# Kernel tuning notes

Hardware: AMD Instinct MI355X
Metric: run time of the kernel (lower is better)

Reference implementation:

```python
import jax, jax.numpy as jnp
import numpy as np
from jax import lax

# constants mirroring init_kwargs
WORD_MIN_SCORE = 0.5
CHAR_MIN_SCORE = 0.25
WORD_STRIDE = 4
CHAR_STRIDE = 4
WORD_NMS_IOU = 0.3
CHAR_NMS_IOU = 0.3
K_WORD = 512   # fixed candidate budget for word NMS (jit-friendly stand-in for dynamic np.where)
K_CHAR = 2048  # fixed candidate budget for char NMS
H_MAP = 512
W_MAP = 512
NUM_CHAR_CLASS = 68


def _oriented_boxes(tblr, orient, scale_w, scale_h, stride):
    # vectorized rotate_rect over every pixel: rect corners (x-l, y-t, x+r, y+b)
    # rotated by angle `orient` around anchor (x, y), all in image coords.
    _, H, W = tblr.shape
    ys, xs = jnp.meshgrid(jnp.arange(H, dtype=tblr.dtype), jnp.arange(W, dtype=tblr.dtype), indexing='ij')
    t, b, l, r = tblr[0], tblr[1], tblr[2], tblr[3]
    sw = scale_w * stride
    sh = scale_h * stride
    x1 = sw * (xs - l); x2 = sw * (xs + r)
    y1 = sh * (ys - t); y2 = sh * (ys + b)
    ax = sw * xs; ay = sh * ys
    cx = jnp.stack([x1, x2, x2, x1], axis=-1)  # [H,W,4]
    cy = jnp.stack([y1, y1, y2, y2], axis=-1)
    c = jnp.cos(orient)[..., None]
    s = jnp.sin(orient)[..., None]
    dx = cx - ax[..., None]
    dy = cy - ay[..., None]
    rx = ax[..., None] + dx * c - dy * s
    ry = ay[..., None] + dx * s + dy * c
    pts = jnp.stack([rx, ry], axis=-1).reshape(H, W, 8)  # x0,y0,...,x3,y3
    return pts.reshape(-1, 8)


def _nms_keep(pts, scores, iou_thresh):
    # pts [K,8] already sorted by descending score; greedy NMS on axis-aligned
    # envelopes of the oriented boxes (fixed-shape stand-in for polygon IoU).
    xs = pts[:, 0::2]; ys = pts[:, 1::2]
    x1 = xs.min(1); x2 = xs.max(1)
    y1 = ys.min(1); y2 = ys.max(1)
    area = jnp.maximum(x2 - x1, 0.0) * jnp.maximum(y2 - y1, 0.0)
    ix1 = jnp.maximum(x1[:, None], x1[None, :])
    iy1 = jnp.maximum(y1[:, None], y1[None, :])
    ix2 = jnp.minimum(x2[:, None], x2[None, :])
    iy2 = jnp.minimum(y2[:, None], y2[None, :])
    inter = jnp.maximum(ix2 - ix1, 0.0) * jnp.maximum(iy2 - iy1, 0.0)
    iou = inter / (area[:, None] + area[None, :] - inter + 1e-6)
    K = pts.shape[0]
    ar = jnp.arange(K)

    def body(i, keep):
        sup = keep[i] & (iou[i] > iou_thresh) & (ar > i)
        return keep & ~sup

    keep = lax.fori_loop(0, K, body, jnp.ones((K,), dtype=bool))
    return keep & (scores > 0.0)


def _clip_round(pts, W, H):
    out = jnp.round(pts)
    x = jnp.clip(out[:, 0::2], 0.0, W - 1.0)
    y = jnp.clip(out[:, 1::2], 0.0, H - 1.0)
    return jnp.stack([x, y], axis=-1).reshape(pts.shape)


def setup_inputs() -> dict:
    key = jax.random.key(0)
    k = jax.random.split(key, 6)
    return {
        'pred_word_fg': jax.random.uniform(k[0], (H_MAP, W_MAP), dtype=jnp.float32),
        'pred_word_tblr': jax.random.uniform(k[1], (4, H_MAP, W_MAP), dtype=jnp.float32) * 4.0,
        'pred_word_orient': jax.random.normal(k[2], (H_MAP, W_MAP), dtype=jnp.float32) * 0.3,
        'pred_char_fg': jax.random.uniform(k[3], (H_MAP, W_MAP), dtype=jnp.float32),
        'pred_char_tblr': jax.random.uniform(k[4], (4, H_MAP, W_MAP), dtype=jnp.float32) * 2.0,
        'pred_char_cls': jax.random.uniform(k[5], (NUM_CHAR_CLASS, H_MAP, W_MAP), dtype=jnp.float32),
        'im_scale_w': 1,
        'im_scale_h': 1,
        'original_im_w': 2048,
        'original_im_h': 2048,
    }


def reference(pred_word_fg, pred_word_tblr, pred_word_orient, pred_char_fg,
              pred_char_tblr, pred_char_cls, im_scale_w, im_scale_h,
              original_im_w, original_im_h):
    sw = float(im_scale_w); sh = float(im_scale_h)
    # ---- parse_word_bboxes ----
    word_pts = _oriented_boxes(pred_word_tblr, pred_word_orient, sw, sh, WORD_STRIDE)
    word_mask = (pred_word_fg > WORD_MIN_SCORE).reshape(-1)
    word_scores = jnp.where(word_mask, pred_word_fg.reshape(-1), 0.0)
    ws, widx = lax.top_k(word_scores, K_WORD)
    wpts = word_pts[widx]
    wkeep = _nms_keep(wpts, ws, WORD_NMS_IOU)
    wpts = _clip_round(wpts, original_im_w, original_im_h)
    word_bboxes = jnp.concatenate([wpts, ws[:, None]], axis=1)  # [K_WORD, 9]
    # ---- parse_char_torch (orientation fixed at 0) ----
    char_pts = _oriented_boxes(pred_char_tblr, jnp.zeros_like(pred_char_fg), sw, sh, CHAR_STRIDE)
    char_mask = word_mask & (pred_char_fg > CHAR_MIN_SCORE).reshape(-1)
    char_fg_scores = jnp.where(char_mask, pred_char_fg.reshape(-1), 0.0)
    cs, cidx = lax.top_k(char_fg_scores, K_CHAR)
    cpts = char_pts[cidx]
    ckeep = _nms_keep(cpts, cs, CHAR_NMS_IOU)
    cpts = _clip_round(cpts, original_im_w, original_im_h)
    char_bboxes = jnp.concatenate([cpts, cs[:, None]], axis=1)  # [K_CHAR, 9]
    C = pred_char_cls.shape[0]
    cls_flat = pred_char_cls.reshape(C, -1).T  # [H*W, C]
    char_scores = cls_flat[cidx]               # [K_CHAR, C]
    return (char_bboxes, char_scores, word_bboxes, wkeep, ckeep)
```

## Files before the change

### kernel.cpp

```cpp
#include <hip/hip_runtime.h>
#include <stdint.h>

typedef unsigned long long u64;
typedef unsigned int u32;

#define N_PIX (512*512)
#define KW 512
#define KC 2048
#define CAPW 4096
#define CAPC 4096
#define NUM_CLS 68
#define WORD_THR 0.5f
#define CHAR_THR 0.25f
#define IOU_THR 0.3f
#define NBLK 128
#define BS 512
#define GSZ (NBLK*BS)
#define LKW 256
#define LKC 256
#define BASE16W 0x3F00u
#define BASE16C 0x3E80u

struct SelState { u64 prefix; u32 kRem; u32 counter; u32 hist[256]; };

__device__ __forceinline__ u64 mk_key(u32 fb, u32 i){
  return (((u64)fb) << 32) | (u64)(0xFFFFFFFFu - i);
}

__global__ void k0_init(SelState* stW, SelState* stC, u32* bars){
  int t = threadIdx.x;
  if (t==0){ stW->prefix=0ull; stW->kRem=KW; stW->counter=0u; }
  if (t==1){ stC->prefix=0ull; stC->kRem=KC; stC->counter=0u; }
  if (t < 8) bars[t] = 0u;
  stW->hist[t]=0u; stC->hist[t]=0u;
}

__device__ __forceinline__ void scan_wave(SelState* st, u32 base16, int lane){
  u32 h[4];
  #pragma unroll
  for (int q=0;q<4;q++)
    h[q] = __hip_atomic_load(&st->hist[lane*4+q], __ATOMIC_RELAXED, __HIP_MEMORY_SCOPE_AGENT);
  u32 lsum = h[0]+h[1]+h[2]+h[3];
  u32 v = lsum;
  #pragma unroll
  for (int off=1; off<64; off<<=1){
    u32 t2 = __shfl_down(v, off, 64);
    if (lane + off < 64) v += t2;
  }
  u32 above = v - lsum;
  u32 k = st->kRem;
  u32 sfx1 = h[3]+h[2]+h[1], sfx2 = h[3]+h[2], sfx3 = h[3];
  int best = -1;
  if      (above + sfx3 >= k) best = lane*4+3;
  else if (above + sfx2 >= k) best = lane*4+2;
  else if (above + sfx1 >= k) best = lane*4+1;
  else if (above + lsum >= k) best = lane*4+0;
  u64 m = __ballot(best >= 0);
  int d = 0;
  if (m != 0ull){
    int hi_lane = 63 - __clzll(m);
    d = __shfl(best, hi_lane, 64);
  }
  if (lane==0)
    __hip_atomic_store(&st->prefix, ((u64)(base16 + (u32)d)) << 48,
                       __ATOMIC_RELAXED, __HIP_MEMORY_SCOPE_AGENT);
}

__global__ __launch_bounds__(BS)
void k1_hist(const float* __restrict__ wfg, const float* __restrict__ cfg,
             SelState* stW, SelState* stC, u32* bars, u32* ranks){
  __shared__ u32 hW[256], hC[256];
  __shared__ int isLast;
  const int tid = threadIdx.x;
  const int gtid = blockIdx.x*BS + tid;
  const int lane = tid & 63;
  if (gtid < CAPW+CAPC) ranks[gtid] = 0u;
  if (tid < 256){ hW[tid]=0u; hC[tid]=0u; }
  __syncthreads();
  float4 wv4 = ((const float4*)wfg)[gtid];
  float4 cv4 = ((const float4*)cfg)[gtid];
  #pragma unroll
  for (int q=0;q<4;q++){
    float wf = q==0?wv4.x:(q==1?wv4.y:(q==2?wv4.z:wv4.w));
    float cf = q==0?cv4.x:(q==1?cv4.y:(q==2?cv4.z:cv4.w));
    bool wp = wf > WORD_THR;
    if (wp) atomicAdd(&hW[(__float_as_uint(wf)>>16) - BASE16W], 1u);
    if (wp && cf > CHAR_THR) atomicAdd(&hC[(__float_as_uint(cf)>>16) - BASE16C], 1u);
  }
  __syncthreads();
  if (tid < 256){
    if (hW[tid]) atomicAdd(&stW->hist[tid], hW[tid]);
    if (hC[tid]) atomicAdd(&stC->hist[tid], hC[tid]);
  }
  __syncthreads();
  if (tid==0){
    u32 p = __hip_atomic_fetch_add(&bars[0],1u,__ATOMIC_ACQ_REL,__HIP_MEMORY_SCOPE_AGENT);
    isLast = (p == NBLK-1);
  }
  __syncthreads();
  if (isLast && tid < 128){
    if (tid < 64) scan_wave(stW, BASE16W, lane);
    else          scan_wave(stC, BASE16C, lane);
  }
}

__global__ __launch_bounds__(BS)
void k2_compact(const float* __restrict__ wfg, const float* __restrict__ cfg,
                SelState* stW, SelState* stC, u64* candW, u64* candC){
  __shared__ u64 lkW[LKW], lkC[LKC];
  __shared__ u32 lcW, lcC, baseW, baseC;
  const int tid = threadIdx.x;
  const int gtid = blockIdx.x*BS + tid;
  const int lane = tid & 63;
  const u64 lmlt = (1ull << lane) - 1ull;
  if (tid==0){ lcW = 0u; lcC = 0u; }
  __syncthreads();
  u64 tW = stW->prefix, tC = stC->prefix;
  float4 wv4 = ((const float4*)wfg)[gtid];
  float4 cv4 = ((const float4*)cfg)[gtid];
  #pragma unroll
  for (int q=0;q<4;q++){
    float wf = q==0?wv4.x:(q==1?wv4.y:(q==2?wv4.z:wv4.w));
    float cf = q==0?cv4.x:(q==1?cv4.y:(q==2?cv4.z:cv4.w));
    u32 i = 4u*(u32)gtid + (u32)q;
    bool wp = wf > WORD_THR;
    u64 kWd = mk_key(__float_as_uint(wf), i);
    bool pw = wp && (kWd >= tW);
    u64 mW = __ballot(pw);
    if (mW){
      u32 base;
      int ldr = __ffsll(mW) - 1;
      if (lane == ldr) base = atomicAdd(&lcW, (u32)__popcll(mW));
      base = __shfl(base, ldr, 64);
      if (pw){ u32 p = base + (u32)__popcll(mW & lmlt); if (p < LKW) lkW[p] = kWd; }
    }
    u64 kCh = mk_key(__float_as_uint(cf), i);
    bool pc = wp && (cf > CHAR_THR) && (kCh >= tC);
    u64 mC = __ballot(pc);
    if (mC){
      u32 base;
      int ldr = __ffsll(mC) - 1;
      if (lane == ldr) base = atomicAdd(&lcC, (u32)__popcll(mC));
      base = __shfl(base, ldr, 64);
      if (pc){ u32 p = base + (u32)__popcll(mC & lmlt); if (p < LKC) lkC[p] = kCh; }
    }
  }
  __syncthreads();
  if (tid==0)      baseW = atomicAdd(&stW->counter, min(lcW,(u32)LKW));
  else if (tid==1) baseC = atomicAdd(&stC->counter, min(lcC,(u32)LKC));
  __syncthreads();
  u32 nW = min(lcW,(u32)LKW), nC = min(lcC,(u32)LKC);
  for (u32 t = tid; t < nW; t += BS){ u32 p = baseW + t; if (p < CAPW) candW[p] = lkW[t]; }
  for (u32 t = tid; t < nC; t += BS){ u32 p = baseC + t; if (p < CAPC) candC[p] = lkC[t]; }
}

__global__ __launch_bounds__(BS)
void k3_rank(SelState* stW, SelState* stC, u64* candW, u64* candC, u32* ranks, u32* bars,
             const float* __restrict__ wtblr, const float* __restrict__ worient,
             const float* __restrict__ ctblr,
             const int* p_sw, const int* p_sh, const int* p_ow, const int* p_oh,
             u64* sortedW, u64* sortedC, float4* aabbW, float4* aabbC,
             float* out_wb, float* out_cb){
  __shared__ u64 chunk[256];
  const int tid = threadIdx.x;
  u32 CW = stW->counter; if (CW > CAPW) CW = CAPW;
  u32 CC = stC->counter; if (CC > CAPC) CC = CAPC;
  bool live = false; bool myW = false; u64 my = 0ull;
  float bx0,bx1,bx2,bx3,bx4,bx5,bx6,bx7,bx8;
  float4 av;
  if (tid < 64){
    int t = blockIdx.x*64 + tid;
    myW = (t < CAPW);
    int slot = myW ? t : t - CAPW;
    u32 C = myW ? CW : CC;
    if (slot < (int)C){
      live = true;
      my = (myW ? candW : candC)[slot];
      u32 idx = 0xFFFFFFFFu - (u32)(my & 0xFFFFFFFFull);
      float score = __uint_as_float((u32)(my>>32));
      float swf = (float)(*p_sw) * 4.0f;
      float shf = (float)(*p_sh) * 4.0f;
      float owm = (float)(*p_ow) - 1.0f, ohm = (float)(*p_oh) - 1.0f;
      const float* tblr = myW ? wtblr : ctblr;
      float tt2 = tblr[idx], bb = tblr[N_PIX+idx], ll = tblr[2*N_PIX+idx], rr = tblr[3*N_PIX+idx];
      float xf = (float)(idx & 511u), yf = (float)(idx >> 9);
      float c = 1.0f, sn = 0.0f;
      if (myW){ float o = worient[idx]; c = cosf(o); sn = sinf(o); }
      float x1 = swf*(xf - ll), x2 = swf*(xf + rr);
      float y1 = shf*(yf - tt2), y2 = shf*(yf + bb);
      float ax = swf*xf, ay = shf*yf;
      float cx[4] = {x1,x2,x2,x1};
      float cy[4] = {y1,y1,y2,y2};
      float rx[4], ry[4];
      #pragma unroll
      for (int q=0;q<4;q++){
        float dx = cx[q]-ax, dy = cy[q]-ay;
        rx[q] = ax + dx*c - dy*sn;
        ry[q] = ay + dx*sn + dy*c;
      }
      float minx = fminf(fminf(rx[0],rx[1]),fminf(rx[2],rx[3]));
      float maxx = fmaxf(fmaxf(rx[0],rx[1]),fmaxf(rx[2],rx[3]));
      float miny = fminf(fminf(ry[0],ry[1]),fminf(ry[2],ry[3]));
      float maxy = fmaxf(fmaxf(ry[0],ry[1]),fmaxf(ry[2],ry[3]));
      av = make_float4(minx,miny,maxx,maxy);
      bx0 = fminf(fmaxf(rintf(rx[0]),0.0f), owm); bx1 = fminf(fmaxf(rintf(ry[0]),0.0f), ohm);
      bx2 = fminf(fmaxf(rintf(rx[1]),0.0f), owm); bx3 = fminf(fmaxf(rintf(ry[1]),0.0f), ohm);
      bx4 = fminf(fmaxf(rintf(rx[2]),0.0f), owm); bx5 = fminf(fmaxf(rintf(ry[2]),0.0f), ohm);
      bx6 = fminf(fmaxf(rintf(rx[3]),0.0f), owm); bx7 = fminf(fmaxf(rintf(ry[3]),0.0f), ohm);
      bx8 = score;
    }
  }
  {
    int gW = (int)((CW + 511) >> 9), hW = (int)((CW + 255) >> 8);
    int gC = (int)((CC + 511) >> 9), hC = (int)((CC + 255) >> 8);
    int tilesW = gW*hW, tiles = tilesW + gC*hC;
    for (int t = blockIdx.x; t < tiles; t += NBLK){
      bool isW = (t < tilesW);
      int tt = isW ? t : t - tilesW;
      int h  = isW ? hW : hC;
      u32 C  = isW ? CW : CC;
      const u64* cand = isW ? candW : candC;
      u32* rk = isW ? ranks : (ranks + CAPW);
      int sg = tt / h, ch = tt - sg*h;
      __syncthreads();
      if (tid < 256){ int ci = ch*256 + tid; chunk[tid] = (ci < (int)C) ? cand[ci] : 0ull; }
      __syncthreads();
      int slot = sg*BS + tid;
      if (slot < (int)C){
        u64 m2 = cand[slot];
        int cnt = 0;
        const ulonglong2* cp = (const ulonglong2*)chunk;
        #pragma unroll 8
        for (int i2=0;i2<128;i2++){ ulonglong2 v = cp[i2]; cnt += (v.x > m2) + (v.y > m2); }
        if (cnt) atomicAdd(&rk[slot], (u32)cnt);
      }
    }
  }
  __syncthreads();
  if (tid==0){
    __hip_atomic_fetch_add(&bars[3],1u,__ATOMIC_ACQ_REL,__HIP_MEMORY_SCOPE_AGENT);
    while (__hip_atomic_load(&bars[3], __ATOMIC_ACQUIRE, __HIP_MEMORY_SCOPE_AGENT) < (u32)NBLK)
      __builtin_amdgcn_s_sleep(2);
  }
  __syncthreads();
  if (live){
    int t = blockIdx.x*64 + tid;
    int rank = (int)ranks[t];
    int K = myW ? KW : KC;
    if (rank < K){
      (myW ? sortedW : sortedC)[rank] = my;
      (myW ? aabbW : aabbC)[rank] = av;
      float* ob = myW ? out_wb : out_cb;
      ob[rank*9+0]=bx0; ob[rank*9+1]=bx1; ob[rank*9+2]=bx2; ob[rank*9+3]=bx3;
      ob[rank*9+4]=bx4; ob[rank*9+5]=bx5; ob[rank*9+6]=bx6; ob[rank*9+7]=bx7;
      ob[rank*9+8]=bx8;
    }
  }
}

template<int W>
__device__ __forceinline__ void sup_row(int j, int lane, const float4* __restrict__ aabb,
                                        u64* __restrict__ supT, u32* __restrict__ rm){
  float4 bj = aabb[j];
  float aj = fmaxf(bj.z-bj.x,0.0f)*fmaxf(bj.w-bj.y,0.0f);
  u32 m = 0;
  #pragma unroll 4
  for (int w=0; w<W; w++){
    int i = w*64 + lane;
    float4 bi = aabb[i];
    float ai = fmaxf(bi.z-bi.x,0.0f)*fmaxf(bi.w-bi.y,0.0f);
    float ix1=fmaxf(bi.x,bj.x), iy1=fmaxf(bi.y,bj.y);
    float ix2=fminf(bi.z,bj.z), iy2=fminf(bi.w,bj.w);
    float inter = fmaxf(ix2-ix1,0.0f)*fmaxf(iy2-iy1,0.0f);
    float iou = inter/(ai+aj-inter+1e-6f);
    bool bit = (iou > IOU_THR) && (i < j);
    u64 b = __ballot(bit);
    if (b){ if (lane==0) supT[(size_t)j*W + w] = b; m |= 1u << w; }
  }
  if (lane==0) rm[j] = m;
}

template<int K, int W>
__device__ void nms_body(u64* kw, int* changed,
                         const u64* __restrict__ supT, const u32* __restrict__ rm,
                         const u64* __restrict__ sorted, float* __restrict__ keep){
  const int tid = threadIdx.x;
  const int lane = tid & 63, wv = tid >> 6;
  constexpr int NB = (K + BS - 1)/BS;
  if (tid < W) kw[tid] = ~0ull;
  __syncthreads();
  for(;;){
    if (tid==0) *changed = 0;
    __syncthreads();
    bool nb[NB];
    #pragma unroll
    for (int q=0;q<NB;q++){
      int j = q*BS + tid;
      bool ok = (j < K);
      u64 su = 0ull;
      if (ok){
        u32 m = rm[j];
        while (m){ int w = __ffs(m)-1; m &= m-1u; su |= supT[(size_t)j*W + w] & kw[w]; }
      }
      nb[q] = ok && (su == 0ull);
    }
    __syncthreads();
    #pragma unroll
    for (int q=0;q<NB;q++){
      int wi = q*(BS/64) + wv;
      u64 b = __ballot(nb[q]);
      if (lane==0 && wi < W){
        if (b != kw[wi]){ kw[wi] = b; *changed = 1; }
      }
    }
    __syncthreads();
    int ch = *changed;
    __syncthreads();
    if (!ch) break;
  }
  #pragma unroll
  for (int q=0;q<NB;q++){
    int j = q*BS + tid;
    if (j < K){
      u64 key = sorted[j];
      bool pos = ((u32)(key>>32)) != 0u;
      bool kp = (((kw[j>>6] >> (j&63)) & 1ull) != 0ull) && pos;
      keep[j] = kp ? 1.0f : 0.0f;
    }
  }
}

__global__ __launch_bounds__(BS)
void k4_tail(const float4* __restrict__ aabbW, const float4* __restrict__ aabbC,
             u64* supTW, u64* supTC, u32* rmW, u32* rmC, u32* bars,
             const u64* __restrict__ sortedW, const u64* __restrict__ sortedC,
             const float* __restrict__ ccls, float* __restrict__ out_cs,
             float* out_wk, float* out_ck){
  __shared__ u64 kw[KC/64];
  __shared__ int changed;
  const int tid = threadIdx.x;
  const int gtid = blockIdx.x*BS + tid;
  const int lane = tid & 63;
  int gw = gtid >> 6;
  for (int row = gw; row < KW+KC; row += GSZ/64){
    if (row < KW) sup_row<KW/64>(row, lane, aabbW, supTW, rmW);
    else          sup_row<KC/64>(row-KW, lane, aabbC, supTC, rmC);
  }
  if (blockIdx.x >= 2){
    for (int t = (blockIdx.x-2)*BS + tid; t < KC*NUM_CLS; t += (NBLK-2)*BS){
      int k = t / NUM_CLS;
      int c = t - k*NUM_CLS;
      u32 idx = 0xFFFFFFFFu - (u32)(sortedC[k] & 0xFFFFFFFFull);
      out_cs[t] = ccls[(size_t)c*N_PIX + idx];
    }
  }
  __syncthreads();
  if (tid==0) __hip_atomic_fetch_add(&bars[2],1u,__ATOMIC_ACQ_REL,__HIP_MEMORY_SCOPE_AGENT);
  if (blockIdx.x >= 2) return;
  if (tid==0){
    while (__hip_atomic_load(&bars[2], __ATOMIC_ACQUIRE, __HIP_MEMORY_SCOPE_AGENT) < (u32)NBLK)
      __builtin_amdgcn_s_sleep(2);
  }
  __syncthreads();
  if (blockIdx.x == 0) nms_body<KW, KW/64>(kw, &changed, supTW, rmW, sortedW, out_wk);
  else                 nms_body<KC, KC/64>(kw, &changed, supTC, rmC, sortedC, out_ck);
}

extern "C" void kernel_launch(void* const* d_in, const int* in_sizes, int n_in,
                              void* d_out, int out_size, void* d_ws, size_t ws_size,
                              hipStream_t stream) {
  const float* wfg     = (const float*)d_in[0];
  const float* wtblr   = (const float*)d_in[1];
  const float* worient = (const float*)d_in[2];
  const float* cfg     = (const float*)d_in[3];
  const float* ctblr   = (const float*)d_in[4];
  const float* ccls    = (const float*)d_in[5];
  const int* p_sw = (const int*)d_in[6];
  const int* p_sh = (const int*)d_in[7];
  const int* p_ow = (const int*)d_in[8];
  const int* p_oh = (const int*)d_in[9];

  char* ws = (char*)d_ws;
  u64* candW   = (u64*)(ws + 0);
  u64* candC   = (u64*)(ws + 32768);
  u64* supTW   = (u64*)(ws + 0);
  u64* supTC   = (u64*)(ws + 32768);
  u32* ranks   = (u32*)(ws + 65536);
  u64* sortedW = (u64*)(ws + 557056);
  u64* sortedC = (u64*)(ws + 561152);
  float4* aabbW= (float4*)(ws + 577536);
  float4* aabbC= (float4*)(ws + 585728);
  u32* rmW     = (u32*)(ws + 618496);
  u32* rmC     = (u32*)(ws + 620544);
  SelState* stW= (SelState*)(ws + 628736);
  u32* bars    = (u32*)(ws + 630016);
  SelState* stC= (SelState*)(ws + 630784);

  float* out = (float*)d_out;
  float* out_cb = out;
  float* out_cs = out + KC*9;
  float* out_wb = out + KC*9 + KC*NUM_CLS;
  float* out_wk = out_wb + KW*9;
  float* out_ck = out_wk + KW;

  k0_init<<<1, 256, 0, stream>>>(stW, stC, bars);
  k1_hist<<<NBLK, BS, 0, stream>>>(wfg, cfg, stW, stC, bars, ranks);
  k2_compact<<<NBLK, BS, 0, stream>>>(wfg, cfg, stW, stC, candW, candC);
  k3_rank<<<NBLK, BS, 0, stream>>>(stW, stC, candW, candC, ranks, bars,
                                   wtblr, worient, ctblr, p_sw, p_sh, p_ow, p_oh,
                                   sortedW, sortedC, aabbW, aabbC, out_wb, out_cb);
  k4_tail<<<NBLK, BS, 0, stream>>>(aabbW, aabbC, supTW, supTC, rmW, rmC, bars,
                                   sortedW, sortedC, ccls, out_cs, out_wk, out_ck);
}
```

Before: 64.63 us.

## Fuse histogram and compaction kernels with grid barrier and LDS key staging

Merges the histogram and compaction passes into one kernel. Each block stages all passing keys in LDS during the histogram pass, waits on a global spin barrier for the last block's threshold scan, then filters its staged keys against the threshold and writes the survivors. The goal is to drop one kernel launch and the second read of both score maps. In exchange, LDS use rises to about 36KB per block, the kernel relies on all 128 blocks being co-resident for the spin barrier, and bars[0] is reused as the flag. The tail kernel also signals its barrier before the class gather so the NMS blocks can start earlier.

```diff
diff --git a/kernel.cpp b/kernel.cpp
--- a/kernel.cpp
+++ b/kernel.cpp
@@ -16,8 +16,6 @@
 #define NBLK 128
 #define BS 512
 #define GSZ (NBLK*BS)
-#define LKW 256
-#define LKC 256
 #define BASE16W 0x3F00u
 #define BASE16C 0x3E80u
 
@@ -67,25 +65,57 @@
 }
 
 __global__ __launch_bounds__(BS)
-void k1_hist(const float* __restrict__ wfg, const float* __restrict__ cfg,
-             SelState* stW, SelState* stC, u32* bars, u32* ranks){
+void k1_histcompact(const float* __restrict__ wfg, const float* __restrict__ cfg,
+                    SelState* stW, SelState* stC, u32* bars, u32* ranks,
+                    u64* candW, u64* candC){
   __shared__ u32 hW[256], hC[256];
+  __shared__ u64 lkW[2048], lkC[2048];
+  __shared__ u64 outW[256], outC[256];
+  __shared__ u32 lcW, lcC, ocW, ocC, baseW, baseC;
   __shared__ int isLast;
   const int tid = threadIdx.x;
   const int gtid = blockIdx.x*BS + tid;
   const int lane = tid & 63;
+  const u64 lmlt = (1ull << lane) - 1ull;
   if (gtid < CAPW+CAPC) ranks[gtid] = 0u;
   if (tid < 256){ hW[tid]=0u; hC[tid]=0u; }
-  __syncthreads();
-  float4 wv4 = ((const float4*)wfg)[gtid];
-  float4 cv4 = ((const float4*)cfg)[gtid];
-  #pragma unroll
-  for (int q=0;q<4;q++){
-    float wf = q==0?wv4.x:(q==1?wv4.y:(q==2?wv4.z:wv4.w));
-    float cf = q==0?cv4.x:(q==1?cv4.y:(q==2?cv4.z:cv4.w));
-    bool wp = wf > WORD_THR;
-    if (wp) atomicAdd(&hW[(__float_as_uint(wf)>>16) - BASE16W], 1u);
-    if (wp && cf > CHAR_THR) atomicAdd(&hC[(__float_as_uint(cf)>>16) - BASE16C], 1u);
+  if (tid==0){ lcW=0u; lcC=0u; ocW=0u; ocC=0u; }
+  __syncthreads();
+  {
+    float4 wv4 = ((const float4*)wfg)[gtid];
+    float4 cv4 = ((const float4*)cfg)[gtid];
+    #pragma unroll
+    for (int q=0;q<4;q++){
+      float wf = q==0?wv4.x:(q==1?wv4.y:(q==2?wv4.z:wv4.w));
+      float cf = q==0?cv4.x:(q==1?cv4.y:(q==2?cv4.z:cv4.w));
+      u32 i = 4u*(u32)gtid + (u32)q;
+      bool wp = wf > WORD_THR;
+      u64 mW = __ballot(wp);
+      if (mW){
+        u32 base;
+        int ldr = __ffsll(mW) - 1;
+        if (lane == ldr) base = atomicAdd(&lcW, (u32)__popcll(mW));
+        base = __shfl(base, ldr, 64);
+        if (wp){
+          u32 fb = __float_as_uint(wf);
+          lkW[base + (u32)__popcll(mW & lmlt)] = mk_key(fb, i);
+          atomicAdd(&hW[(fb>>16) - BASE16W], 1u);
+        }
+      }
+      bool cp = wp && (cf > CHAR_THR);
+      u64 mC = __ballot(cp);
+      if (mC){
+        u32 base;
+        int ldr = __ffsll(mC) - 1;
+        if (lane == ldr) base = atomicAdd(&lcC, (u32)__popcll(mC));
+        base = __shfl(base, ldr, 64);
+        if (cp){
+          u32 fb = __float_as_uint(cf);
+          lkC[base + (u32)__popcll(mC & lmlt)] = mk_key(fb, i);
+          atomicAdd(&hC[(fb>>16) - BASE16C], 1u);
+        }
+      }
+    }
   }
   __syncthreads();
   if (tid < 256){
@@ -98,60 +128,61 @@
     isLast = (p == NBLK-1);
   }
   __syncthreads();
-  if (isLast && tid < 128){
-    if (tid < 64) scan_wave(stW, BASE16W, lane);
-    else          scan_wave(stC, BASE16C, lane);
-  }
-}
-
-__global__ __launch_bounds__(BS)
-void k2_compact(const float* __restrict__ wfg, const float* __restrict__ cfg,
-                SelState* stW, SelState* stC, u64* candW, u64* candC){
-  __shared__ u64 lkW[LKW], lkC[LKC];
-  __shared__ u32 lcW, lcC, baseW, baseC;
-  const int tid = threadIdx.x;
-  const int gtid = blockIdx.x*BS + tid;
-  const int lane = tid & 63;
-  const u64 lmlt = (1ull << lane) - 1ull;
-  if (tid==0){ lcW = 0u; lcC = 0u; }
-  __syncthreads();
-  u64 tW = stW->prefix, tC = stC->prefix;
-  float4 wv4 = ((const float4*)wfg)[gtid];
-  float4 cv4 = ((const float4*)cfg)[gtid];
-  #pragma unroll
-  for (int q=0;q<4;q++){
-    float wf = q==0?wv4.x:(q==1?wv4.y:(q==2?wv4.z:wv4.w));
-    float cf = q==0?cv4.x:(q==1?cv4.y:(q==2?cv4.z:cv4.w));
-    u32 i = 4u*(u32)gtid + (u32)q;
-    bool wp = wf > WORD_THR;
-    u64 kWd = mk_key(__float_as_uint(wf), i);
-    bool pw = wp && (kWd >= tW);
-    u64 mW = __ballot(pw);
-    if (mW){
-      u32 base;
-      int ldr = __ffsll(mW) - 1;
-      if (lane == ldr) base = atomicAdd(&lcW, (u32)__popcll(mW));
-      base = __shfl(base, ldr, 64);
-      if (pw){ u32 p = base + (u32)__popcll(mW & lmlt); if (p < LKW) lkW[p] = kWd; }
-    }
-    u64 kCh = mk_key(__float_as_uint(cf), i);
-    bool pc = wp && (cf > CHAR_THR) && (kCh >= tC);
-    u64 mC = __ballot(pc);
-    if (mC){
-      u32 base;
-      int ldr = __ffsll(mC) - 1;
-      if (lane == ldr) base = atomicAdd(&lcC, (u32)__popcll(mC));
-      base = __shfl(base, ldr, 64);
-      if (pc){ u32 p = base + (u32)__popcll(mC & lmlt); if (p < LKC) lkC[p] = kCh; }
-    }
-  }
-  __syncthreads();
-  if (tid==0)      baseW = atomicAdd(&stW->counter, min(lcW,(u32)LKW));
-  else if (tid==1) baseC = atomicAdd(&stC->counter, min(lcC,(u32)LKC));
-  __syncthreads();
-  u32 nW = min(lcW,(u32)LKW), nC = min(lcC,(u32)LKC);
-  for (u32 t = tid; t < nW; t += BS){ u32 p = baseW + t; if (p < CAPW) candW[p] = lkW[t]; }
-  for (u32 t = tid; t < nC; t += BS){ u32 p = baseC + t; if (p < CAPC) candC[p] = lkC[t]; }
+  if (isLast){
+    if (tid < 128){
+      if (tid < 64) scan_wave(stW, BASE16W, lane);
+      else          scan_wave(stC, BASE16C, lane);
+    }
+    __syncthreads();
+    if (tid==0)
+      __hip_atomic_store(&bars[0], 0xFFFFFFFFu, __ATOMIC_RELEASE, __HIP_MEMORY_SCOPE_AGENT);
+  } else if (tid==0){
+    while (__hip_atomic_load(&bars[0], __ATOMIC_ACQUIRE, __HIP_MEMORY_SCOPE_AGENT) != 0xFFFFFFFFu)
+      __builtin_amdgcn_s_sleep(2);
+  }
+  __syncthreads();
+  {
+    u64 tW = __hip_atomic_load(&stW->prefix, __ATOMIC_RELAXED, __HIP_MEMORY_SCOPE_AGENT);
+    u64 tC = __hip_atomic_load(&stC->prefix, __ATOMIC_RELAXED, __HIP_MEMORY_SCOPE_AGENT);
+    u32 nW = lcW, nC = lcC;
+    for (u32 b = 0; b < nW; b += BS){
+      u32 t = b + tid;
+      bool act = (t < nW);
+      u64 k = act ? lkW[t] : 0ull;
+      bool pw = act && (k >= tW);
+      u64 m = __ballot(pw);
+      if (m){
+        u32 base;
+        int ldr = __ffsll(m) - 1;
+        if (lane == ldr) base = atomicAdd(&ocW, (u32)__popcll(m));
+        base = __shfl(base, ldr, 64);
+        if (pw){ u32 p = base + (u32)__popcll(m & lmlt); if (p < 256) outW[p] = k; }
+      }
+    }
+    for (u32 b = 0; b < nC; b += BS){
+      u32 t = b + tid;
+      bool act = (t < nC);
+      u64 k = act ? lkC[t] : 0ull;
+      bool pc = act && (k >= tC);
+      u64 m = __ballot(pc);
+      if (m){
+        u32 base;
+        int ldr = __ffsll(m) - 1;
+        if (lane == ldr) base = atomicAdd(&ocC, (u32)__popcll(m));
+        base = __shfl(base, ldr, 64);
+        if (pc){ u32 p = base + (u32)__popcll(m & lmlt); if (p < 256) outC[p] = k; }
+      }
+    }
+  }
+  __syncthreads();
+  if (tid==0)      baseW = atomicAdd(&stW->counter, min(ocW,256u));
+  else if (tid==1) baseC = atomicAdd(&stC->counter, min(ocC,256u));
+  __syncthreads();
+  {
+    u32 nW = min(ocW,256u), nC = min(ocC,256u);
+    for (u32 t = tid; t < nW; t += BS){ u32 p = baseW + t; if (p < CAPW) candW[p] = outW[t]; }
+    for (u32 t = tid; t < nC; t += BS){ u32 p = baseC + t; if (p < CAPC) candC[p] = outC[t]; }
+  }
 }
 
 __global__ __launch_bounds__(BS)
@@ -346,6 +377,8 @@
     if (row < KW) sup_row<KW/64>(row, lane, aabbW, supTW, rmW);
     else          sup_row<KC/64>(row-KW, lane, aabbC, supTC, rmC);
   }
+  __syncthreads();
+  if (tid==0) __hip_atomic_fetch_add(&bars[2],1u,__ATOMIC_ACQ_REL,__HIP_MEMORY_SCOPE_AGENT);
   if (blockIdx.x >= 2){
     for (int t = (blockIdx.x-2)*BS + tid; t < KC*NUM_CLS; t += (NBLK-2)*BS){
       int k = t / NUM_CLS;
@@ -353,10 +386,8 @@
       u32 idx = 0xFFFFFFFFu - (u32)(sortedC[k] & 0xFFFFFFFFull);
       out_cs[t] = ccls[(size_t)c*N_PIX + idx];
     }
-  }
-  __syncthreads();
-  if (tid==0) __hip_atomic_fetch_add(&bars[2],1u,__ATOMIC_ACQ_REL,__HIP_MEMORY_SCOPE_AGENT);
-  if (blockIdx.x >= 2) return;
+    return;
+  }
   if (tid==0){
     while (__hip_atomic_load(&bars[2], __ATOMIC_ACQUIRE, __HIP_MEMORY_SCOPE_AGENT) < (u32)NBLK)
       __builtin_amdgcn_s_sleep(2);
@@ -404,8 +435,7 @@
   float* out_ck = out_wk + KW;
 
   k0_init<<<1, 256, 0, stream>>>(stW, stC, bars);
-  k1_hist<<<NBLK, BS, 0, stream>>>(wfg, cfg, stW, stC, bars, ranks);
-  k2_compact<<<NBLK, BS, 0, stream>>>(wfg, cfg, stW, stC, candW, candC);
+  k1_histcompact<<<NBLK, BS, 0, stream>>>(wfg, cfg, stW, stC, bars, ranks, candW, candC);
   k3_rank<<<NBLK, BS, 0, stream>>>(stW, stC, candW, candC, ranks, bars,
                                    wtblr, worient, ctblr, p_sw, p_sh, p_ow, p_oh,
                                    sortedW, sortedC, aabbW, aabbC, out_wb, out_cb);
```

Measured after the change: 67.80 us. 4.9% more time.
